# Kernel optimization log

Measured on AMD Instinct MI355X. Metric: run time of the kernel, lower is better.

## Reference

```python
import jax, jax.numpy as jnp
import numpy as np

N_EMBD = 1024
N_HEAD = 16
B, T = 2, 2048


def setup_inputs() -> dict:
    key = jax.random.key(0)
    k1, k2, k3 = jax.random.split(key, 3)
    scale = 1.0 / np.sqrt(N_EMBD)
    x = jax.random.normal(k1, (B, T, N_EMBD), dtype=jnp.float32)
    W_qkv = jax.random.normal(k2, (N_EMBD, 3 * N_EMBD), dtype=jnp.float32) * scale
    b_qkv = jnp.zeros((3 * N_EMBD,), dtype=jnp.float32)
    W_proj = jax.random.normal(k3, (N_EMBD, N_EMBD), dtype=jnp.float32) * scale
    b_proj = jnp.zeros((N_EMBD,), dtype=jnp.float32)
    return {"x": x, "W_qkv": W_qkv, "b_qkv": b_qkv, "W_proj": W_proj, "b_proj": b_proj}


def reference(x, W_qkv, b_qkv, W_proj, b_proj):
    Bx, Tx, C = x.shape
    H = N_HEAD
    D = C // H  # head_size
    qkv = x @ W_qkv + b_qkv  # [B,T,3C]
    Q, K, V = jnp.split(qkv, 3, axis=2)
    # [B,T,C] -> [B,H,T,D]
    Q = Q.reshape(Bx, Tx, H, D).transpose(0, 2, 1, 3)
    K = K.reshape(Bx, Tx, H, D).transpose(0, 2, 1, 3)
    V = V.reshape(Bx, Tx, H, D).transpose(0, 2, 1, 3)
    scores = jnp.einsum("bhqd,bhkd->bhqk", Q, K) / jnp.sqrt(jnp.float32(D))
    causal = jnp.tril(jnp.ones((Tx, Tx), dtype=bool))
    scores = jnp.where(causal, scores, jnp.float32(-jnp.inf))
    weights = jax.nn.softmax(scores, axis=-1)
    out = jnp.einsum("bhqk,bhkd->bhqd", weights, V)  # [B,H,T,D]
    out = out.transpose(0, 2, 1, 3).reshape(Bx, Tx, C)
    return out @ W_proj + b_proj
```

## Files before the change

### kernel.cpp

```cpp
#include <hip/hip_runtime.h>
#include <hip/hip_bf16.h>
#include <math.h>

#define BB 2
#define TT 2048
#define CC 1024
#define HH 16
#define DD 64
#define C3 3072
#define BT 4096

typedef __attribute__((ext_vector_type(8))) short short8;
typedef __attribute__((ext_vector_type(8))) unsigned short ushort8;
typedef __attribute__((ext_vector_type(4))) unsigned short ushort4v;
typedef __attribute__((ext_vector_type(4))) float floatx4;

__device__ __forceinline__ unsigned short f2b(float f) {
    union { float f; unsigned int u; } v; v.f = f;
    unsigned int u = v.u;
    unsigned int r = (u + 0x7fffu + ((u >> 16) & 1u)) >> 16;
    return (unsigned short)r;
}
__device__ __forceinline__ unsigned short f2b_fast(float f) {
    unsigned int u = __builtin_bit_cast(unsigned int, f);
    return (unsigned short)((u + 0x8000u) >> 16);
}

__device__ __forceinline__ void store_out(unsigned short* p, float v) { *p = f2b(v); }
__device__ __forceinline__ void store_out(float* p, float v) { *p = v; }

__device__ __forceinline__ void async16(const unsigned short* g, unsigned short* lds) {
    __builtin_amdgcn_global_load_lds(
        (const __attribute__((address_space(1))) unsigned int*)g,
        (__attribute__((address_space(3))) unsigned int*)lds, 16, 0, 0);
}

__global__ __launch_bounds__(256) void prep_kernel(
    const float* __restrict__ x, unsigned short* __restrict__ xb,
    const float* __restrict__ Wqkv, const float* __restrict__ Wproj,
    unsigned short* __restrict__ Wqkv_t, unsigned short* __restrict__ Wproj_t)
{
    __shared__ float tile[64 * 65];
    const int tid = threadIdx.x;
    const int bid = blockIdx.x;

    if (bid < 2048) {
        int i = bid * 256 + tid;
        const float4 v0 = *(const float4*)&x[(size_t)i * 8];
        const float4 v1 = *(const float4*)&x[(size_t)i * 8 + 4];
        ushort8 pk;
        pk[0] = f2b(v0.x); pk[1] = f2b(v0.y); pk[2] = f2b(v0.z); pk[3] = f2b(v0.w);
        pk[4] = f2b(v1.x); pk[5] = f2b(v1.y); pk[6] = f2b(v1.z); pk[7] = f2b(v1.w);
        *(ushort8*)&xb[(size_t)i * 8] = pk;
        return;
    }

    const int xt = bid - 2048;
    const int cxt = xt & 63;
    const int r0  = (xt >> 6) * 64;
    const float* src; unsigned short* dst; int Ccols, c0;
    if (cxt < 48) { src = Wqkv;  dst = Wqkv_t;  Ccols = C3; c0 = cxt * 64; }
    else          { src = Wproj; dst = Wproj_t; Ccols = CC; c0 = (cxt - 48) * 64; }
#pragma unroll
    for (int it = 0; it < 4; it++) {
        int idx = it * 256 + tid;
        int row = idx >> 4;
        int c4  = idx & 15;
        float4 v = *(const float4*)&src[(size_t)(r0 + row) * Ccols + c0 + c4 * 4];
        tile[row * 65 + c4 * 4 + 0] = v.x;
        tile[row * 65 + c4 * 4 + 1] = v.y;
        tile[row * 65 + c4 * 4 + 2] = v.z;
        tile[row * 65 + c4 * 4 + 3] = v.w;
    }
    __syncthreads();
#pragma unroll
    for (int it = 0; it < 2; it++) {
        int idx = it * 256 + tid;
        int orow = idx >> 3;
        int o8   = idx & 7;
        ushort8 pk;
#pragma unroll
        for (int j = 0; j < 8; j++) pk[j] = f2b(tile[(o8 * 8 + j) * 65 + orow]);
        *(ushort8*)&dst[(size_t)(c0 + orow) * CC + r0 + o8 * 8] = pk;
    }
}

template <typename OUT_T, bool WVT>
__global__ __launch_bounds__(256) void gemm_bt_kernel(
    const unsigned short* __restrict__ A, const unsigned short* __restrict__ Bm,
    const float* __restrict__ bias, OUT_T* __restrict__ Cmat,
    unsigned short* __restrict__ Vt,
    int M, int N, int K, float qscale, int qcols)
{
    __shared__ __align__(16) unsigned short sA[128 * 64];
    __shared__ __align__(16) unsigned short sB[128 * 64];

    const int tid = threadIdx.x;
    const int lane16 = tid & 15, quad = (tid & 63) >> 4;
    const int w = tid >> 6;
    const int wm = w >> 1, wn = w & 1;
    const int m0 = blockIdx.y * 128, n0 = blockIdx.x * 128;
    const int lx = lane16 & 7;

    floatx4 acc[4][4] = {};

    for (int kt = 0; kt < K; kt += 64) {
#pragma unroll
        for (int it = 0; it < 4; it++) {
            int idx = it * 256 + tid;
            int row = idx >> 3;
            int c8m = (idx & 7) ^ (row & 7);
            int wslot = it * 256 + (tid & 192);
            async16(&A[(size_t)(m0 + row) * K + kt + c8m * 8], &sA[wslot * 8]);
            async16(&Bm[(size_t)(n0 + row) * K + kt + c8m * 8], &sB[wslot * 8]);
        }
        __syncthreads();
#pragma unroll
        for (int ks = 0; ks < 64; ks += 32) {
            const int slot = ((ks >> 3) + quad) ^ lx;
            short8 af[4], bf[4];
#pragma unroll
            for (int t = 0; t < 4; t++) {
                af[t] = *(const short8*)&sA[(wm * 64 + t * 16 + lane16) * 64 + slot * 8];
                bf[t] = *(const short8*)&sB[(wn * 64 + t * 16 + lane16) * 64 + slot * 8];
            }
#pragma unroll
            for (int mt = 0; mt < 4; mt++)
#pragma unroll
                for (int nt = 0; nt < 4; nt++)
                    acc[mt][nt] = __builtin_amdgcn_mfma_f32_16x16x32_bf16(
                        af[mt], bf[nt], acc[mt][nt], 0, 0, 0);
        }
        __syncthreads();
    }

#pragma unroll
    for (int mt = 0; mt < 4; mt++) {
#pragma unroll
        for (int nt = 0; nt < 4; nt++) {
            int col = n0 + wn * 64 + nt * 16 + lane16;
            float bv = bias[col];
            float sc = (col < qcols) ? qscale : 1.0f;
            float v[4];
            int row0 = m0 + wm * 64 + mt * 16 + quad * 4;
#pragma unroll
            for (int r = 0; r < 4; r++) {
                v[r] = (acc[mt][nt][r] + bv) * sc;
                store_out(&Cmat[(size_t)(row0 + r) * N + col], v[r]);
            }
            if (WVT && n0 >= 2 * CC) {
                int hd = col - 2 * CC;
                int b  = row0 >> 11;
                int token = row0 & (TT - 1);
                ushort4v pk;
#pragma unroll
                for (int r = 0; r < 4; r++) pk[r] = f2b(v[r]);
                *(ushort4v*)&Vt[((size_t)(b * HH * DD) + hd) * TT + token] = pk;
            }
        }
    }
}

__global__ __launch_bounds__(256) void attn_mfma_kernel(
    const unsigned short* __restrict__ qkv, const unsigned short* __restrict__ Vt,
    unsigned short* __restrict__ att)
{
    __shared__ __align__(16) unsigned short Ks[64 * 72];
    __shared__ __align__(16) unsigned short Vs[64 * 72];
    __shared__ __align__(16) unsigned short Pl[64 * 76];

    const int tid = threadIdx.x;
    const int l = tid & 63;
    const int lane16 = l & 15, quad = l >> 4;
    const int w = tid >> 6;
    const int bh = blockIdx.x;
    const int b = bh >> 4, h = bh & 15;

    const int y = blockIdx.y;
    const int gcu = y & 7, s = y >> 3;
    const int p = 8 * s + ((s & 1) ? (7 - gcu) : gcu);

    const int srow = tid >> 3;
    const int sc8  = (tid & 7) * 8;
    const unsigned short* kbase = &qkv[(size_t)(b * TT) * C3 + CC + h * DD + sc8];
    const unsigned short* vbase = &Vt[(size_t)(bh * DD + srow) * TT + sc8];

    const int q0 = p * 64;
    const int qw = q0 + w * 16;

    short8 qf[2];
    {
        const unsigned short* qp =
            &qkv[(size_t)(b * TT + qw + lane16) * C3 + h * DD + quad * 8];
        qf[0] = *(const short8*)&qp[0];
        qf[1] = *(const short8*)&qp[32];
    }

    float psum[4] = {0.f, 0.f, 0.f, 0.f};
    floatx4 O[4] = {};

    ushort8 kr0 = *(const ushort8*)&kbase[(size_t)srow * C3];
    ushort8 kr1 = *(const ushort8*)&kbase[(size_t)(srow + 32) * C3];
    ushort8 vr0 = *(const ushort8*)&vbase[0];
    ushort8 vr1 = *(const ushort8*)&vbase[(size_t)32 * TT];

    const int ntiles = p + 1;
    for (int t = 0; t < ntiles; ++t) {
        const int k0 = t * 64;
        __syncthreads();
        *(ushort8*)&Ks[srow * 72 + sc8]        = kr0;
        *(ushort8*)&Ks[(srow + 32) * 72 + sc8] = kr1;
        *(ushort8*)&Vs[srow * 72 + sc8]        = vr0;
        *(ushort8*)&Vs[(srow + 32) * 72 + sc8] = vr1;
        __syncthreads();

        if (t + 1 < ntiles) {
            const int kn = k0 + 64;
            kr0 = *(const ushort8*)&kbase[(size_t)(kn + srow) * C3];
            kr1 = *(const ushort8*)&kbase[(size_t)(kn + srow + 32) * C3];
            vr0 = *(const ushort8*)&vbase[kn];
            vr1 = *(const ushort8*)&vbase[(size_t)32 * TT + kn];
        }

        floatx4 s4[4] = {};
#pragma unroll
        for (int nt = 0; nt < 4; nt++) {
            short8 kf0 = *(const short8*)&Ks[(nt * 16 + lane16) * 72 + quad * 8];
            short8 kf1 = *(const short8*)&Ks[(nt * 16 + lane16) * 72 + 32 + quad * 8];
            s4[nt] = __builtin_amdgcn_mfma_f32_16x16x32_bf16(qf[0], kf0, s4[nt], 0, 0, 0);
            s4[nt] = __builtin_amdgcn_mfma_f32_16x16x32_bf16(qf[1], kf1, s4[nt], 0, 0, 0);
        }

        if (t == ntiles - 1) {
#pragma unroll
            for (int nt = 0; nt < 4; nt++) {
                int key = k0 + nt * 16 + lane16;
#pragma unroll
                for (int r = 0; r < 4; r++) {
                    float v = (key > qw + quad * 4 + r) ? -1e30f : s4[nt][r];
                    float pe = __builtin_amdgcn_exp2f(v);
                    psum[r] += pe;
                    Pl[(w * 16 + quad * 4 + r) * 76 + nt * 16 + lane16] = f2b_fast(pe);
                }
            }
        } else {
#pragma unroll
            for (int nt = 0; nt < 4; nt++) {
#pragma unroll
                for (int r = 0; r < 4; r++) {
                    float pe = __builtin_amdgcn_exp2f(s4[nt][r]);
                    psum[r] += pe;
                    Pl[(w * 16 + quad * 4 + r) * 76 + nt * 16 + lane16] = f2b_fast(pe);
                }
            }
        }
        __threadfence_block();

        short8 pf0 = *(const short8*)&Pl[(w * 16 + lane16) * 76 + quad * 8];
        short8 pf1 = *(const short8*)&Pl[(w * 16 + lane16) * 76 + 32 + quad * 8];
#pragma unroll
        for (int dt = 0; dt < 4; dt++) {
            short8 vf0 = *(const short8*)&Vs[(dt * 16 + lane16) * 72 + quad * 8];
            short8 vf1 = *(const short8*)&Vs[(dt * 16 + lane16) * 72 + 32 + quad * 8];
            O[dt] = __builtin_amdgcn_mfma_f32_16x16x32_bf16(pf0, vf0, O[dt], 0, 0, 0);
            O[dt] = __builtin_amdgcn_mfma_f32_16x16x32_bf16(pf1, vf1, O[dt], 0, 0, 0);
        }
    }

#pragma unroll
    for (int off = 1; off <= 8; off <<= 1)
#pragma unroll
        for (int r = 0; r < 4; r++)
            psum[r] += __shfl_xor(psum[r], off, 64);

    float rl[4];
#pragma unroll
    for (int r = 0; r < 4; r++) rl[r] = 1.0f / psum[r];
#pragma unroll
    for (int dt = 0; dt < 4; dt++)
#pragma unroll
        for (int r = 0; r < 4; r++) {
            int qq = qw + quad * 4 + r;
            int d = dt * 16 + lane16;
            att[(size_t)(b * TT + qq) * CC + h * DD + d] = f2b(O[dt][r] * rl[r]);
        }
}

extern "C" void kernel_launch(void* const* d_in, const int* in_sizes, int n_in,
                              void* d_out, int out_size, void* d_ws, size_t ws_size,
                              hipStream_t stream) {
    const float* x     = (const float*)d_in[0];
    const float* Wqkv  = (const float*)d_in[1];
    const float* bqkv  = (const float*)d_in[2];
    const float* Wproj = (const float*)d_in[3];
    const float* bproj = (const float*)d_in[4];
    float* out = (float*)d_out;

    unsigned short* xb      = (unsigned short*)d_ws;
    unsigned short* qkv_b   = xb      + (size_t)BT * CC;
    unsigned short* Wqkv_t  = qkv_b   + (size_t)BT * C3;
    unsigned short* Wproj_t = Wqkv_t  + (size_t)C3 * CC;
    unsigned short* Vt      = Wproj_t + (size_t)CC * CC;
    unsigned short* att_b   = Vt      + (size_t)BB * HH * DD * TT;

    prep_kernel<<<3072, 256, 0, stream>>>(x, xb, Wqkv, Wproj, Wqkv_t, Wproj_t);

    {
        dim3 grid(C3 / 128, BT / 128);
        gemm_bt_kernel<unsigned short, true><<<grid, 256, 0, stream>>>(
            xb, Wqkv_t, bqkv, qkv_b, Vt, BT, C3, CC, 0.125f * 1.44269504f, CC);
    }
    {
        dim3 grid(BB * HH, 32);
        attn_mfma_kernel<<<grid, 256, 0, stream>>>(qkv_b, Vt, att_b);
    }
    {
        dim3 grid(CC / 128, BT / 128);
        gemm_bt_kernel<float, false><<<grid, 256, 0, stream>>>(
            att_b, Wproj_t, bproj, out, nullptr, BT, CC, CC, 1.0f, 0);
    }
}
```

Measured before the change: 184.2 us.

## Keep softmax probabilities in registers via transposed QK^T and double-buffer K/V LDS

```diff
diff --git a/kernel.cpp b/kernel.cpp
--- a/kernel.cpp
+++ b/kernel.cpp
@@ -11,6 +11,7 @@
 #define BT 4096
 
 typedef __attribute__((ext_vector_type(8))) short short8;
+typedef __attribute__((ext_vector_type(4))) short short4v;
 typedef __attribute__((ext_vector_type(8))) unsigned short ushort8;
 typedef __attribute__((ext_vector_type(4))) unsigned short ushort4v;
 typedef __attribute__((ext_vector_type(4))) float floatx4;
@@ -165,9 +166,8 @@
     const unsigned short* __restrict__ qkv, const unsigned short* __restrict__ Vt,
     unsigned short* __restrict__ att)
 {
-    __shared__ __align__(16) unsigned short Ks[64 * 72];
-    __shared__ __align__(16) unsigned short Vs[64 * 72];
-    __shared__ __align__(16) unsigned short Pl[64 * 76];
+    __shared__ __align__(16) unsigned short Ks[2][64 * 72];
+    __shared__ __align__(16) unsigned short Vs[2][64 * 72];
 
     const int tid = threadIdx.x;
     const int l = tid & 63;
@@ -196,7 +196,7 @@
         qf[1] = *(const short8*)&qp[32];
     }
 
-    float psum[4] = {0.f, 0.f, 0.f, 0.f};
+    float ps = 0.f;
     floatx4 O[4] = {};
 
     ushort8 kr0 = *(const ushort8*)&kbase[(size_t)srow * C3];
@@ -207,11 +207,14 @@
     const int ntiles = p + 1;
     for (int t = 0; t < ntiles; ++t) {
         const int k0 = t * 64;
-        __syncthreads();
-        *(ushort8*)&Ks[srow * 72 + sc8]        = kr0;
-        *(ushort8*)&Ks[(srow + 32) * 72 + sc8] = kr1;
-        *(ushort8*)&Vs[srow * 72 + sc8]        = vr0;
-        *(ushort8*)&Vs[(srow + 32) * 72 + sc8] = vr1;
+        const int cur = t & 1;
+        unsigned short* Kc = (unsigned short*)Ks[cur];
+        unsigned short* Vc = (unsigned short*)Vs[cur];
+
+        *(ushort8*)&Kc[srow * 72 + sc8]        = kr0;
+        *(ushort8*)&Kc[(srow + 32) * 72 + sc8] = kr1;
+        *(ushort8*)&Vc[srow * 72 + sc8]        = vr0;
+        *(ushort8*)&Vc[(srow + 32) * 72 + sc8] = vr1;
         __syncthreads();
 
         if (t + 1 < ntiles) {
@@ -225,22 +228,23 @@
         floatx4 s4[4] = {};
 #pragma unroll
         for (int nt = 0; nt < 4; nt++) {
-            short8 kf0 = *(const short8*)&Ks[(nt * 16 + lane16) * 72 + quad * 8];
-            short8 kf1 = *(const short8*)&Ks[(nt * 16 + lane16) * 72 + 32 + quad * 8];
-            s4[nt] = __builtin_amdgcn_mfma_f32_16x16x32_bf16(qf[0], kf0, s4[nt], 0, 0, 0);
-            s4[nt] = __builtin_amdgcn_mfma_f32_16x16x32_bf16(qf[1], kf1, s4[nt], 0, 0, 0);
-        }
-
+            short8 kf0 = *(const short8*)&Kc[(nt * 16 + lane16) * 72 + quad * 8];
+            short8 kf1 = *(const short8*)&Kc[(nt * 16 + lane16) * 72 + 32 + quad * 8];
+            s4[nt] = __builtin_amdgcn_mfma_f32_16x16x32_bf16(kf0, qf[0], s4[nt], 0, 0, 0);
+            s4[nt] = __builtin_amdgcn_mfma_f32_16x16x32_bf16(kf1, qf[1], s4[nt], 0, 0, 0);
+        }
+
+        short8 pa[2];
         if (t == ntiles - 1) {
 #pragma unroll
             for (int nt = 0; nt < 4; nt++) {
-                int key = k0 + nt * 16 + lane16;
 #pragma unroll
                 for (int r = 0; r < 4; r++) {
-                    float v = (key > qw + quad * 4 + r) ? -1e30f : s4[nt][r];
+                    int key = k0 + nt * 16 + quad * 4 + r;
+                    float v = (key > qw + lane16) ? -1e30f : s4[nt][r];
                     float pe = __builtin_amdgcn_exp2f(v);
-                    psum[r] += pe;
-                    Pl[(w * 16 + quad * 4 + r) * 76 + nt * 16 + lane16] = f2b_fast(pe);
+                    ps += pe;
+                    pa[nt >> 1][(nt & 1) * 4 + r] = (short)f2b_fast(pe);
                 }
             }
         } else {
@@ -249,40 +253,40 @@
 #pragma unroll
                 for (int r = 0; r < 4; r++) {
                     float pe = __builtin_amdgcn_exp2f(s4[nt][r]);
-                    psum[r] += pe;
-                    Pl[(w * 16 + quad * 4 + r) * 76 + nt * 16 + lane16] = f2b_fast(pe);
+                    ps += pe;
+                    pa[nt >> 1][(nt & 1) * 4 + r] = (short)f2b_fast(pe);
                 }
             }
         }
-        __threadfence_block();
-
-        short8 pf0 = *(const short8*)&Pl[(w * 16 + lane16) * 76 + quad * 8];
-        short8 pf1 = *(const short8*)&Pl[(w * 16 + lane16) * 76 + 32 + quad * 8];
+
 #pragma unroll
         for (int dt = 0; dt < 4; dt++) {
-            short8 vf0 = *(const short8*)&Vs[(dt * 16 + lane16) * 72 + quad * 8];
-            short8 vf1 = *(const short8*)&Vs[(dt * 16 + lane16) * 72 + 32 + quad * 8];
-            O[dt] = __builtin_amdgcn_mfma_f32_16x16x32_bf16(pf0, vf0, O[dt], 0, 0, 0);
-            O[dt] = __builtin_amdgcn_mfma_f32_16x16x32_bf16(pf1, vf1, O[dt], 0, 0, 0);
-        }
-    }
-
-#pragma unroll
-    for (int off = 1; off <= 8; off <<= 1)
-#pragma unroll
-        for (int r = 0; r < 4; r++)
-            psum[r] += __shfl_xor(psum[r], off, 64);
-
-    float rl[4];
-#pragma unroll
-    for (int r = 0; r < 4; r++) rl[r] = 1.0f / psum[r];
+            const unsigned short* vrow = &Vc[(dt * 16 + lane16) * 72 + quad * 4];
+            short4v v00 = *(const short4v*)&vrow[0];
+            short4v v01 = *(const short4v*)&vrow[16];
+            short4v v10 = *(const short4v*)&vrow[32];
+            short4v v11 = *(const short4v*)&vrow[48];
+            short8 vf0 = __builtin_shufflevector(v00, v01, 0, 1, 2, 3, 4, 5, 6, 7);
+            short8 vf1 = __builtin_shufflevector(v10, v11, 0, 1, 2, 3, 4, 5, 6, 7);
+            O[dt] = __builtin_amdgcn_mfma_f32_16x16x32_bf16(pa[0], vf0, O[dt], 0, 0, 0);
+            O[dt] = __builtin_amdgcn_mfma_f32_16x16x32_bf16(pa[1], vf1, O[dt], 0, 0, 0);
+        }
+    }
+
+    ps += __shfl_xor(ps, 16, 64);
+    ps += __shfl_xor(ps, 32, 64);
+
+    float rlv[4];
+#pragma unroll
+    for (int r = 0; r < 4; r++) rlv[r] = 1.0f / __shfl(ps, quad * 4 + r, 64);
+
 #pragma unroll
     for (int dt = 0; dt < 4; dt++)
 #pragma unroll
         for (int r = 0; r < 4; r++) {
             int qq = qw + quad * 4 + r;
             int d = dt * 16 + lane16;
-            att[(size_t)(b * TT + qq) * CC + h * DD + d] = f2b(O[dt][r] * rl[r]);
+            att[(size_t)(b * TT + qq) * CC + h * DD + d] = f2b(O[dt][r] * rlv[r]);
         }
 }
 
```

Result: no change. 182.8 us (-0.8%).

## Emit Q/K/V in MFMA fragment layout and run single-wave attention without LDS

Applied to the files above, without the earlier changes.

```diff
diff --git a/kernel.cpp b/kernel.cpp
--- a/kernel.cpp
+++ b/kernel.cpp
@@ -85,12 +85,13 @@
     }
 }
 
-template <typename OUT_T, bool WVT>
+template <typename OUT_T, bool FRAG>
 __global__ __launch_bounds__(256) void gemm_bt_kernel(
     const unsigned short* __restrict__ A, const unsigned short* __restrict__ Bm,
     const float* __restrict__ bias, OUT_T* __restrict__ Cmat,
-    unsigned short* __restrict__ Vt,
-    int M, int N, int K, float qscale, int qcols)
+    unsigned short* __restrict__ Qf, unsigned short* __restrict__ Kf,
+    unsigned short* __restrict__ Vf,
+    int M, int N, int K, float qscale)
 {
     __shared__ __align__(16) unsigned short sA[128 * 64];
     __shared__ __align__(16) unsigned short sB[128 * 64];
@@ -140,149 +141,149 @@
         for (int nt = 0; nt < 4; nt++) {
             int col = n0 + wn * 64 + nt * 16 + lane16;
             float bv = bias[col];
-            float sc = (col < qcols) ? qscale : 1.0f;
-            float v[4];
             int row0 = m0 + wm * 64 + mt * 16 + quad * 4;
-#pragma unroll
-            for (int r = 0; r < 4; r++) {
-                v[r] = (acc[mt][nt][r] + bv) * sc;
-                store_out(&Cmat[(size_t)(row0 + r) * N + col], v[r]);
+            if (!FRAG) {
+#pragma unroll
+                for (int r = 0; r < 4; r++)
+                    store_out(&Cmat[(size_t)(row0 + r) * N + col], acc[mt][nt][r] + bv);
+            } else {
+                const int breg = row0 >> 11;
+                const int tok0 = row0 & (TT - 1);
+                if (col < CC) {
+                    int h = col >> 6, d = col & 63;
+                    int bh = breg * HH + h;
+                    size_t base = ((size_t)(bh * 128 + (tok0 >> 4)) * 2 + (d >> 5)) * 512
+                                + ((d >> 3) & 3) * 128 + (tok0 & 15) * 8 + (d & 7);
+#pragma unroll
+                    for (int r = 0; r < 4; r++)
+                        Qf[base + r * 8] = f2b((acc[mt][nt][r] + bv) * qscale);
+                } else if (col < 2 * CC) {
+                    int c = col - CC;
+                    int h = c >> 6, d = c & 63;
+                    int bh = breg * HH + h;
+                    size_t base = ((size_t)(bh * 128 + (tok0 >> 4)) * 2 + (d >> 5)) * 512
+                                + ((d >> 3) & 3) * 128 + (tok0 & 15) * 8 + (d & 7);
+#pragma unroll
+                    for (int r = 0; r < 4; r++)
+                        Kf[base + r * 8] = f2b(acc[mt][nt][r] + bv);
+                } else {
+                    int c = col - 2 * CC;
+                    int h = c >> 6, d = c & 63;
+                    int bh = breg * HH + h;
+                    size_t base = ((size_t)(bh * 64 + (tok0 >> 5)) * 4 + (d >> 4)) * 512
+                                + (((tok0 >> 2) & 3) * 16 + (d & 15)) * 8
+                                + ((tok0 >> 4) & 1) * 4;
+                    ushort4v pk;
+#pragma unroll
+                    for (int r = 0; r < 4; r++) pk[r] = f2b(acc[mt][nt][r] + bv);
+                    *(ushort4v*)&Vf[base] = pk;
+                }
             }
-            if (WVT && n0 >= 2 * CC) {
-                int hd = col - 2 * CC;
-                int b  = row0 >> 11;
-                int token = row0 & (TT - 1);
-                ushort4v pk;
-#pragma unroll
-                for (int r = 0; r < 4; r++) pk[r] = f2b(v[r]);
-                *(ushort4v*)&Vt[((size_t)(b * HH * DD) + hd) * TT + token] = pk;
-            }
-        }
-    }
-}
-
-__global__ __launch_bounds__(256) void attn_mfma_kernel(
-    const unsigned short* __restrict__ qkv, const unsigned short* __restrict__ Vt,
-    unsigned short* __restrict__ att)
+        }
+    }
+}
+
+__global__ __launch_bounds__(64) void attn_mfma_kernel(
+    const unsigned short* __restrict__ Qf, const unsigned short* __restrict__ Kf,
+    const unsigned short* __restrict__ Vf, unsigned short* __restrict__ att)
 {
-    __shared__ __align__(16) unsigned short Ks[64 * 72];
-    __shared__ __align__(16) unsigned short Vs[64 * 72];
-    __shared__ __align__(16) unsigned short Pl[64 * 76];
-
-    const int tid = threadIdx.x;
-    const int l = tid & 63;
+    const int l = threadIdx.x;
     const int lane16 = l & 15, quad = l >> 4;
-    const int w = tid >> 6;
     const int bh = blockIdx.x;
     const int b = bh >> 4, h = bh & 15;
 
     const int y = blockIdx.y;
     const int gcu = y & 7, s = y >> 3;
     const int p = 8 * s + ((s & 1) ? (7 - gcu) : gcu);
-
-    const int srow = tid >> 3;
-    const int sc8  = (tid & 7) * 8;
-    const unsigned short* kbase = &qkv[(size_t)(b * TT) * C3 + CC + h * DD + sc8];
-    const unsigned short* vbase = &Vt[(size_t)(bh * DD + srow) * TT + sc8];
-
     const int q0 = p * 64;
-    const int qw = q0 + w * 16;
-
-    short8 qf[2];
-    {
-        const unsigned short* qp =
-            &qkv[(size_t)(b * TT + qw + lane16) * C3 + h * DD + quad * 8];
-        qf[0] = *(const short8*)&qp[0];
-        qf[1] = *(const short8*)&qp[32];
-    }
-
-    float psum[4] = {0.f, 0.f, 0.f, 0.f};
-    floatx4 O[4] = {};
-
-    ushort8 kr0 = *(const ushort8*)&kbase[(size_t)srow * C3];
-    ushort8 kr1 = *(const ushort8*)&kbase[(size_t)(srow + 32) * C3];
-    ushort8 vr0 = *(const ushort8*)&vbase[0];
-    ushort8 vr1 = *(const ushort8*)&vbase[(size_t)32 * TT];
+
+    const unsigned short* Qb = Qf + (size_t)bh * 131072 + l * 8;
+    const unsigned short* Kb = Kf + (size_t)bh * 131072 + l * 8;
+    const unsigned short* Vb = Vf + (size_t)bh * 131072 + l * 8;
+
+    short8 qf[4][2];
+#pragma unroll
+    for (int qg = 0; qg < 4; qg++)
+#pragma unroll
+        for (int dc = 0; dc < 2; dc++)
+            qf[qg][dc] = *(const short8*)&Qb[(size_t)((p * 4 + qg) * 2 + dc) * 512];
+
+    floatx4 O[4][4] = {};
+    float ps[4] = {0.f, 0.f, 0.f, 0.f};
+    short8 kfa[8], kfb[8];
 
     const int ntiles = p + 1;
-    for (int t = 0; t < ntiles; ++t) {
-        const int k0 = t * 64;
-        __syncthreads();
-        *(ushort8*)&Ks[srow * 72 + sc8]        = kr0;
-        *(ushort8*)&Ks[(srow + 32) * 72 + sc8] = kr1;
-        *(ushort8*)&Vs[srow * 72 + sc8]        = vr0;
-        *(ushort8*)&Vs[(srow + 32) * 72 + sc8] = vr1;
-        __syncthreads();
+#pragma unroll
+    for (int i = 0; i < 8; i++)
+        kfa[i] = *(const short8*)&Kb[(size_t)i * 512];
+
+    auto body = [&](int t, short8 (&KC)[8], short8 (&KN)[8]) {
+        const bool last = (t == ntiles - 1);
+
+        short8 vf[8];
+#pragma unroll
+        for (int i = 0; i < 8; i++)
+            vf[i] = *(const short8*)&Vb[(size_t)(t * 8 + i) * 512];
 
         if (t + 1 < ntiles) {
-            const int kn = k0 + 64;
-            kr0 = *(const ushort8*)&kbase[(size_t)(kn + srow) * C3];
-            kr1 = *(const ushort8*)&kbase[(size_t)(kn + srow + 32) * C3];
-            vr0 = *(const ushort8*)&vbase[kn];
-            vr1 = *(const ushort8*)&vbase[(size_t)32 * TT + kn];
-        }
-
-        floatx4 s4[4] = {};
+#pragma unroll
+            for (int i = 0; i < 8; i++)
+                KN[i] = *(const short8*)&Kb[(size_t)((t + 1) * 8 + i) * 512];
+        }
+
+        short8 pa[4][2];
 #pragma unroll
         for (int nt = 0; nt < 4; nt++) {
-            short8 kf0 = *(const short8*)&Ks[(nt * 16 + lane16) * 72 + quad * 8];
-            short8 kf1 = *(const short8*)&Ks[(nt * 16 + lane16) * 72 + 32 + quad * 8];
-            s4[nt] = __builtin_amdgcn_mfma_f32_16x16x32_bf16(qf[0], kf0, s4[nt], 0, 0, 0);
-            s4[nt] = __builtin_amdgcn_mfma_f32_16x16x32_bf16(qf[1], kf1, s4[nt], 0, 0, 0);
-        }
-
-        if (t == ntiles - 1) {
-#pragma unroll
-            for (int nt = 0; nt < 4; nt++) {
-                int key = k0 + nt * 16 + lane16;
+#pragma unroll
+            for (int qg = 0; qg < 4; qg++) {
+                floatx4 s4 = {};
+                s4 = __builtin_amdgcn_mfma_f32_16x16x32_bf16(KC[nt * 2 + 0], qf[qg][0], s4, 0, 0, 0);
+                s4 = __builtin_amdgcn_mfma_f32_16x16x32_bf16(KC[nt * 2 + 1], qf[qg][1], s4, 0, 0, 0);
 #pragma unroll
                 for (int r = 0; r < 4; r++) {
-                    float v = (key > qw + quad * 4 + r) ? -1e30f : s4[nt][r];
+                    float v = s4[r];
+                    if (last) {
+                        if (nt * 16 + quad * 4 + r > qg * 16 + lane16) v = -1e30f;
+                    }
                     float pe = __builtin_amdgcn_exp2f(v);
-                    psum[r] += pe;
-                    Pl[(w * 16 + quad * 4 + r) * 76 + nt * 16 + lane16] = f2b_fast(pe);
+                    ps[qg] += pe;
+                    pa[qg][nt >> 1][(nt & 1) * 4 + r] = (short)f2b_fast(pe);
                 }
             }
-        } else {
-#pragma unroll
-            for (int nt = 0; nt < 4; nt++) {
-#pragma unroll
-                for (int r = 0; r < 4; r++) {
-                    float pe = __builtin_amdgcn_exp2f(s4[nt][r]);
-                    psum[r] += pe;
-                    Pl[(w * 16 + quad * 4 + r) * 76 + nt * 16 + lane16] = f2b_fast(pe);
-                }
-            }
-        }
-        __threadfence_block();
-
-        short8 pf0 = *(const short8*)&Pl[(w * 16 + lane16) * 76 + quad * 8];
-        short8 pf1 = *(const short8*)&Pl[(w * 16 + lane16) * 76 + 32 + quad * 8];
-#pragma unroll
-        for (int dt = 0; dt < 4; dt++) {
-            short8 vf0 = *(const short8*)&Vs[(dt * 16 + lane16) * 72 + quad * 8];
-            short8 vf1 = *(const short8*)&Vs[(dt * 16 + lane16) * 72 + 32 + quad * 8];
-            O[dt] = __builtin_amdgcn_mfma_f32_16x16x32_bf16(pf0, vf0, O[dt], 0, 0, 0);
-            O[dt] = __builtin_amdgcn_mfma_f32_16x16x32_bf16(pf1, vf1, O[dt], 0, 0, 0);
-        }
-    }
-
-#pragma unroll
-    for (int off = 1; off <= 8; off <<= 1)
-#pragma unroll
-        for (int r = 0; r < 4; r++)
-            psum[r] += __shfl_xor(psum[r], off, 64);
-
-    float rl[4];
-#pragma unroll
-    for (int r = 0; r < 4; r++) rl[r] = 1.0f / psum[r];
-#pragma unroll
-    for (int dt = 0; dt < 4; dt++)
+        }
+
+#pragma unroll
+        for (int kc = 0; kc < 2; kc++)
+#pragma unroll
+            for (int dt = 0; dt < 4; dt++)
+#pragma unroll
+                for (int qg = 0; qg < 4; qg++)
+                    O[qg][dt] = __builtin_amdgcn_mfma_f32_16x16x32_bf16(
+                        pa[qg][kc], vf[kc * 4 + dt], O[qg][dt], 0, 0, 0);
+    };
+
+    int t = 0;
+    while (true) {
+        body(t, kfa, kfb); if (++t == ntiles) break;
+        body(t, kfb, kfa); if (++t == ntiles) break;
+    }
+
+#pragma unroll
+    for (int qg = 0; qg < 4; qg++) {
+        ps[qg] += __shfl_xor(ps[qg], 16, 64);
+        ps[qg] += __shfl_xor(ps[qg], 32, 64);
+    }
+
+    unsigned short* ob = att + ((size_t)(b * TT) + q0) * CC + h * DD;
+#pragma unroll
+    for (int qg = 0; qg < 4; qg++)
 #pragma unroll
         for (int r = 0; r < 4; r++) {
-            int qq = qw + quad * 4 + r;
-            int d = dt * 16 + lane16;
-            att[(size_t)(b * TT + qq) * CC + h * DD + d] = f2b(O[dt][r] * rl[r]);
+            float rl = 1.0f / __shfl(ps[qg], quad * 4 + r, 16);
+            int q = qg * 16 + quad * 4 + r;
+#pragma unroll
+            for (int dt = 0; dt < 4; dt++)
+                ob[(size_t)q * CC + dt * 16 + lane16] = f2b(O[qg][dt][r] * rl);
         }
 }
 
@@ -296,27 +297,31 @@
     const float* bproj = (const float*)d_in[4];
     float* out = (float*)d_out;
 
+    const size_t FRAG_ELEMS = (size_t)128 * 2 * 512;
     unsigned short* xb      = (unsigned short*)d_ws;
-    unsigned short* qkv_b   = xb      + (size_t)BT * CC;
-    unsigned short* Wqkv_t  = qkv_b   + (size_t)BT * C3;
-    unsigned short* Wproj_t = Wqkv_t  + (size_t)C3 * CC;
-    unsigned short* Vt      = Wproj_t + (size_t)CC * CC;
-    unsigned short* att_b   = Vt      + (size_t)BB * HH * DD * TT;
+    unsigned short* Qf      = xb + (size_t)BT * CC;
+    unsigned short* Kf      = Qf + (size_t)BB * HH * FRAG_ELEMS;
+    unsigned short* Vf      = Kf + (size_t)BB * HH * FRAG_ELEMS;
+    unsigned short* Wqkv_t  = Vf + (size_t)BB * HH * FRAG_ELEMS;
+    unsigned short* Wproj_t = Wqkv_t + (size_t)C3 * CC;
+    unsigned short* att_b   = Wproj_t + (size_t)CC * CC;
 
     prep_kernel<<<3072, 256, 0, stream>>>(x, xb, Wqkv, Wproj, Wqkv_t, Wproj_t);
 
     {
         dim3 grid(C3 / 128, BT / 128);
         gemm_bt_kernel<unsigned short, true><<<grid, 256, 0, stream>>>(
-            xb, Wqkv_t, bqkv, qkv_b, Vt, BT, C3, CC, 0.125f * 1.44269504f, CC);
+            xb, Wqkv_t, bqkv, (unsigned short*)nullptr, Qf, Kf, Vf,
+            BT, C3, CC, 0.125f * 1.44269504f);
     }
     {
         dim3 grid(BB * HH, 32);
-        attn_mfma_kernel<<<grid, 256, 0, stream>>>(qkv_b, Vt, att_b);
+        attn_mfma_kernel<<<grid, 64, 0, stream>>>(Qf, Kf, Vf, att_b);
     }
     {
         dim3 grid(CC / 128, BT / 128);
         gemm_bt_kernel<float, false><<<grid, 256, 0, stream>>>(
-            att_b, Wproj_t, bproj, out, nullptr, BT, CC, CC, 1.0f, 0);
-    }
-}
+            att_b, Wproj_t, bproj, out, nullptr, nullptr, nullptr,
+            BT, CC, CC, 1.0f);
+    }
+}
```

New measurement: 194.8 us. 5.7% more time.
